# Optimization experiments

Hardware: AMD Instinct MI355X
Metric: run time of the kernel (lower is better)

## Reference

```python
import jax, jax.numpy as jnp
import numpy as np

B, T, C = 8, 2048, 1024
HS = 128           # head_size
N_TERMS = 2
THETA = 10000.0


def _rope_tables(dim, end):
    freqs = 1.0 / (THETA ** (jnp.arange(0, dim, 2, dtype=jnp.float32) / dim))  # [dim/2]
    ang = jnp.arange(end, dtype=jnp.float32)[:, None] * freqs[None, :]          # [end, dim/2]
    return jnp.cos(ang), jnp.sin(ang)


def _apply_rope(x, cos, sin):
    # x: [..., T, D]; pairs are interleaved (x0,x1),(x2,x3),...
    xr = x[..., 0::2]
    xi = x[..., 1::2]
    or_ = xr * cos - xi * sin
    oi = xr * sin + xi * cos
    return jnp.stack([or_, oi], axis=-1).reshape(x.shape)


def setup_inputs() -> dict:
    key = jax.random.key(0)
    ks = jax.random.split(key, 6)
    x = jax.random.normal(ks[0], (B, T, C), dtype=jnp.float32)
    Wq = jax.random.normal(ks[1], (N_TERMS, C, HS), dtype=jnp.float32) * 0.02
    Wk = jax.random.normal(ks[2], (N_TERMS, C, HS), dtype=jnp.float32) * 0.02
    Wv = jax.random.normal(ks[3], (C, 2 * HS), dtype=jnp.float32) * 0.02
    lambda_q = jax.random.normal(ks[4], (N_TERMS, HS), dtype=jnp.float32) * 0.1
    lambda_k = jax.random.normal(ks[5], (N_TERMS, HS), dtype=jnp.float32) * 0.1
    return {"x": x, "Wq": Wq, "Wk": Wk, "Wv": Wv,
            "lambda_q": lambda_q, "lambda_k": lambda_k, "layer_idx": 3}


def reference(x, Wq, Wk, Wv, lambda_q, lambda_k, layer_idx):
    Bx, Tx, Cx = x.shape
    n = Wq.shape[0]
    scale = 1.0 / (HS ** 0.5)

    v = x @ Wv                                   # [B,T,2*HS]
    q = jnp.einsum('btc,ncd->nbtd', x, Wq)       # [n,B,T,HS]
    k = jnp.einsum('btc,ncd->nbtd', x, Wk)

    cos, sin = _rope_tables(HS, Tx)              # [T, HS/2]
    q = _apply_rope(q, cos, sin)
    k = _apply_rope(k, cos, sin)

    att = jnp.einsum('nbtd,nbsd->nbts', q, k) * scale  # [n,B,T,T]
    causal = jnp.tril(jnp.ones((Tx, Tx), dtype=bool))
    att = jnp.where(causal, att, -jnp.inf)
    att = jax.nn.softmax(att, axis=-1)

    # lambda values
    lam_init = 0.8 - 0.6 * jnp.exp(-0.3 * (jnp.float32(layer_idx) - 1.0))
    e = jnp.mean(jnp.exp(lambda_q * lambda_k), axis=-1)         # [n]
    e_prev = jnp.concatenate([jnp.zeros((1,), e.dtype), e[:-1]])
    lam = e - e_prev + lam_init                                 # [n]
    signs = jnp.where(jnp.arange(n) % 2 == 1, -1.0, 1.0)

    diff_att = jnp.einsum('n,nbts->bts', signs * lam, att)      # [B,T,T]
    out = diff_att @ v                                          # [B,T,2*HS]
    return out
```

## Files before the change

### kernel.cpp

```cpp
#include <hip/hip_runtime.h>
#include <math.h>

#define B_DIM 8
#define T_DIM 2048
#define C_DIM 1024
#define HS_DIM 128
#define VD 256
#define M_DIM (B_DIM * T_DIM)
#define QK_ELEMS (M_DIM * HS_DIM)
#define SCALE 0.088388347648318447f
#define LOG_THETA 9.210340371976184f

#define QB_OFF   0u
#define KB_OFF   4194304u
#define VT_OFF   8388608u
#define WT_OFF   12582912u
#define XBH_OFF  13369344u
#define LAM_OFF  21757952u
#define XSPLIT_ELEMS 8388608u

typedef short s8v   __attribute__((ext_vector_type(8)));
typedef float f32x4 __attribute__((ext_vector_type(4)));
typedef float f32x16 __attribute__((ext_vector_type(16)));

__device__ __forceinline__ unsigned int bf16_rne(float f) {
    unsigned int u = __float_as_uint(f);
    return (u + 0x7fffu + ((u >> 16) & 1u)) >> 16;
}
__device__ __forceinline__ unsigned int pack_bf2(float lo, float hi) {
    return bf16_rne(lo) | (bf16_rne(hi) << 16);
}
__device__ __forceinline__ void async_cp16(const unsigned short* g, unsigned short* l) {
    __builtin_amdgcn_global_load_lds(
        (const __attribute__((address_space(1))) unsigned int*)g,
        (__attribute__((address_space(3))) unsigned int*)l, 16, 0, 0);
}

__global__ void lam_kernel(const float* __restrict__ lq, const float* __restrict__ lk,
                           const int* __restrict__ lidx, float* __restrict__ lam_out) {
    int t = threadIdx.x;
    float s0 = expf(lq[t] * lk[t]) + expf(lq[t + 64] * lk[t + 64]);
    float s1 = expf(lq[128 + t] * lk[128 + t]) + expf(lq[192 + t] * lk[192 + t]);
    #pragma unroll
    for (int off = 32; off > 0; off >>= 1) {
        s0 += __shfl_down(s0, off);
        s1 += __shfl_down(s1, off);
    }
    if (t == 0) {
        float e0 = s0 * (1.0f / 128.0f);
        float e1 = s1 * (1.0f / 128.0f);
        float li = 0.8f - 0.6f * expf(-0.3f * ((float)lidx[0] - 1.0f));
        lam_out[0] = e0 + li;
        lam_out[1] = -(e1 - e0 + li);
    }
}

__global__ __launch_bounds__(256) void cast_x_kernel(const float* __restrict__ x,
                                                     unsigned short* __restrict__ lo,
                                                     unsigned short* __restrict__ hi) {
    const size_t i8 = ((size_t)blockIdx.x * 256 + threadIdx.x) * 8;
    float4 a = *(const float4*)(x + i8);
    float4 b = *(const float4*)(x + i8 + 4);
    uint4 u;
    u.x = pack_bf2(a.x, a.y); u.y = pack_bf2(a.z, a.w);
    u.z = pack_bf2(b.x, b.y); u.w = pack_bf2(b.z, b.w);
    unsigned short* dst = (i8 < XSPLIT_ELEMS) ? (lo + i8) : (hi + (i8 - XSPLIT_ELEMS));
    *(uint4*)dst = u;
}

__global__ __launch_bounds__(256) void cast_wt_kernel(
    const float* __restrict__ Wq, const float* __restrict__ Wk,
    const float* __restrict__ Wv, unsigned short* __restrict__ wt) {
    __shared__ float tile[32][33];
    const int t = threadIdx.x;
    const int n0 = blockIdx.x * 32;
    const int k0 = blockIdx.y * 32;
    const int seg = n0 >> 7;
    const int nl = t & 31;
    const int ng = n0 + nl;
    const float* src; int ld;
    if (seg < 2)      { src = Wq + (size_t)seg * (C_DIM * HS_DIM) + (ng & 127); ld = 128; }
    else if (seg < 4) { src = Wk + (size_t)(seg - 2) * (C_DIM * HS_DIM) + (ng & 127); ld = 128; }
    else              { src = Wv + (ng - 512); ld = 256; }
    #pragma unroll
    for (int rep = 0; rep < 4; ++rep) {
        int kl = (t >> 5) + rep * 8;
        tile[kl][nl] = src[(size_t)(k0 + kl) * ld];
    }
    __syncthreads();
    unsigned int* wt32 = (unsigned int*)wt;
    #pragma unroll
    for (int rep = 0; rep < 2; ++rep) {
        int nl2 = (t >> 4) + rep * 16;
        int k2 = (t & 15) * 2;
        unsigned int u = pack_bf2(tile[k2][nl2], tile[k2 + 1][nl2]);
        wt32[((size_t)(n0 + nl2) * 1024 + k0 + k2) >> 1] = u;
    }
}

__global__ __launch_bounds__(256) void gemm_kernel(
    const unsigned short* __restrict__ xlo, const unsigned short* __restrict__ xhi,
    const unsigned short* __restrict__ wt,
    unsigned short* __restrict__ qo, unsigned short* __restrict__ ko,
    unsigned short* __restrict__ vo) {
    __shared__ unsigned short As[128 * 32];
    __shared__ unsigned short Bs[128 * 32];

    const int t = threadIdx.x;
    const int wv = t >> 6, lane = t & 63;
    const int quad = lane >> 4, l15 = lane & 15;
    const int m0 = blockIdx.x * 128;
    const int n0 = blockIdx.y * 128;
    const int wr = wv >> 1, wc = wv & 1;

    const unsigned short* xbase = (m0 < 8192)
        ? (xlo + (size_t)m0 * C_DIM) : (xhi + (size_t)(m0 - 8192) * C_DIM);

    f32x4 acc[4][4];
    #pragma unroll
    for (int i = 0; i < 4; ++i)
        #pragma unroll
        for (int j = 0; j < 4; ++j) acc[i][j] = (f32x4){0.f, 0.f, 0.f, 0.f};

    const int srow = lane >> 2;
    const int skof = (lane & 3) * 8;

    for (int k0 = 0; k0 < C_DIM; k0 += 32) {
        #pragma unroll
        for (int j = 0; j < 2; ++j) {
            const int c = wv * 2 + j;
            async_cp16(xbase + (size_t)(c * 16 + srow) * C_DIM + k0 + skof, As + c * 512);
        }
        #pragma unroll
        for (int j = 0; j < 2; ++j) {
            const int c = wv * 2 + j;
            async_cp16(wt + (size_t)(n0 + c * 16 + srow) * C_DIM + k0 + skof, Bs + c * 512);
        }
        __syncthreads();
        s8v af[4], bf[4];
        #pragma unroll
        for (int i = 0; i < 4; ++i)
            af[i] = *(const s8v*)&As[(wr * 64 + i * 16 + l15) * 32 + quad * 8];
        #pragma unroll
        for (int j = 0; j < 4; ++j)
            bf[j] = *(const s8v*)&Bs[(wc * 64 + j * 16 + l15) * 32 + quad * 8];
        #pragma unroll
        for (int i = 0; i < 4; ++i)
            #pragma unroll
            for (int j = 0; j < 4; ++j)
                acc[i][j] = __builtin_amdgcn_mfma_f32_16x16x32_bf16(af[i], bf[j], acc[i][j], 0, 0, 0);
        __syncthreads();
    }

    const int seg = n0 >> 7;
    if (seg < 4) {
        unsigned short* dstbuf = ((seg < 2) ? qo : ko) + (size_t)(seg & 1) * QK_ELEMS;
        float freqj[4];
        #pragma unroll
        for (int j = 0; j < 4; ++j) {
            const int d = wc * 64 + j * 16 + l15;
            freqj[j] = __expf((float)(d >> 1) * (-LOG_THETA / 64.f));
        }
        const int odd = lane & 1;
        #pragma unroll
        for (int i = 0; i < 4; ++i) {
            #pragma unroll
            for (int e = 0; e < 4; ++e) {
                const int m = m0 + wr * 64 + i * 16 + quad * 4 + e;
                const float trow = (float)(m & (T_DIM - 1));
                unsigned int* p32 = (unsigned int*)(dstbuf + (size_t)m * HS_DIM);
                #pragma unroll
                for (int j = 0; j < 4; ++j) {
                    const int d = wc * 64 + j * 16 + l15;
                    const float val = acc[i][j][e];
                    const float other = __shfl_xor(val, 1);
                    float sn_, cs_;
                    __sincosf(trow * freqj[j], &sn_, &cs_);
                    const float out = val * cs_ + (odd ? other * sn_ : -other * sn_);
                    const float out2 = __shfl_xor(out, 1);
                    if (!odd) p32[d >> 1] = pack_bf2(out, out2);
                }
            }
        }
    } else {
        const int bq = m0 >> 11;
        const int tbase = m0 & (T_DIM - 1);
        unsigned int* vT32 = (unsigned int*)vo;
        #pragma unroll
        for (int j = 0; j < 4; ++j) {
            const int d = (seg - 4) * 128 + wc * 64 + j * 16 + l15;
            const size_t rowbase = (size_t)(bq * VD + d) * (T_DIM / 2);
            #pragma unroll
            for (int i = 0; i < 4; ++i) {
                const int tok = tbase + wr * 64 + i * 16 + quad * 4;
                uint2 u;
                u.x = pack_bf2(acc[i][j][0], acc[i][j][1]);
                u.y = pack_bf2(acc[i][j][2], acc[i][j][3]);
                *(uint2*)&vT32[rowbase + (tok >> 1)] = u;
            }
        }
    }
}

#define KSTR 136
#define VSTR 72
#define PSTR 72
#define OSTR 260
#define K_OFF 0
#define V_OFF 34816
#define P_OFF 71680
#define SM_TOTAL 80896

__global__ __launch_bounds__(256, 2) void attn_kernel(
    const unsigned short* __restrict__ qg, const unsigned short* __restrict__ kg,
    const unsigned short* __restrict__ vg, const float* __restrict__ lam,
    float* __restrict__ outp) {
    __shared__ __align__(16) unsigned char smem[SM_TOTAL];
    unsigned short* Ks = (unsigned short*)(smem + K_OFF);
    unsigned short* Vt = (unsigned short*)(smem + V_OFF);
    unsigned short* Ps = (unsigned short*)(smem + P_OFF);
    float* Ol = (float*)smem;
    float* Lsum = (float*)(smem + P_OFF);

    const int t = threadIdx.x;
    const int id = blockIdx.x;
    const int b = id & 7;
    const int sidx = id >> 3;
    const int strip = (sidx < 32) ? (63 - sidx) : (sidx - 32);
    const int q0 = strip * 32;
    const int nt = (strip >> 1) + 1;

    const int w = t >> 6, lane = t & 63;
    const int l31 = lane & 31, lh = lane >> 5;
    const int term = w & 1;
    const int kh = w >> 1;

    const float cn = lam[term];

    const unsigned short* qrow = qg
        + ((size_t)(term * B_DIM + b) * T_DIM + q0 + l31) * HS_DIM + lh * 8;
    s8v qa[8];
    #pragma unroll
    for (int ks = 0; ks < 8; ++ks)
        qa[ks] = *(const s8v*)(qrow + ks * 16);

    f32x16 o[4];
    #pragma unroll
    for (int dt = 0; dt < 4; ++dt)
        #pragma unroll
        for (int r = 0; r < 16; ++r) o[dt][r] = 0.f;
    float l_acc[16];
    #pragma unroll
    for (int r = 0; r < 16; ++r) l_acc[r] = 0.f;

    for (int it = 0; it < nt; ++it) {
        const int s0 = it * 64;
        #pragma unroll
        for (int rep = 0; rep < 8; ++rep) {
            int idx = t + rep * 256;
            int n = idx >> 10, rem = idx & 1023;
            int r = rem >> 4, seg = rem & 15;
            const uint4 g = *(const uint4*)(kg
                + ((size_t)(n * B_DIM + b) * T_DIM + s0 + r) * HS_DIM + seg * 8);
            *(uint4*)&Ks[(n * 64 + r) * KSTR + seg * 8] = g;
        }
        #pragma unroll
        for (int rep = 0; rep < 8; ++rep) {
            int idx = t + rep * 256;
            int d = idx >> 3, seg = idx & 7;
            const uint4 g = *(const uint4*)(vg
                + ((size_t)(b * VD + d) * T_DIM + s0) + seg * 8);
            *(uint4*)&Vt[d * VSTR + seg * 8] = g;
        }
        __syncthreads();

        f32x16 sc;
        #pragma unroll
        for (int r = 0; r < 16; ++r) sc[r] = 0.f;
        #pragma unroll
        for (int ks = 0; ks < 8; ++ks) {
            s8v kf = *(const s8v*)&Ks[(term * 64 + kh * 32 + l31) * KSTR
                                      + ks * 16 + lh * 8];
            sc = __builtin_amdgcn_mfma_f32_32x32x16_bf16(qa[ks], kf, sc, 0, 0, 0);
        }
        const int key = s0 + kh * 32 + l31;
        #pragma unroll
        for (int r = 0; r < 16; ++r) {
            const int row = (r & 3) + 8 * (r >> 2) + 4 * lh;
            const float p = (key <= q0 + row) ? __expf(sc[r] * SCALE) : 0.f;
            l_acc[r] += p;
            Ps[(term * 32 + row) * PSTR + kh * 32 + l31] = (unsigned short)bf16_rne(p);
        }
        __syncthreads();

        #pragma unroll
        for (int ks = 0; ks < 4; ++ks) {
            s8v pa = *(const s8v*)&Ps[(term * 32 + l31) * PSTR + ks * 16 + lh * 8];
            #pragma unroll
            for (int dt = 0; dt < 4; ++dt) {
                s8v vb = *(const s8v*)&Vt[(kh * 128 + dt * 32 + l31) * VSTR
                                          + ks * 16 + lh * 8];
                o[dt] = __builtin_amdgcn_mfma_f32_32x32x16_bf16(pa, vb, o[dt], 0, 0, 0);
            }
        }
        __syncthreads();
    }

    #pragma unroll
    for (int r = 0; r < 16; ++r) {
        float lt = l_acc[r];
        #pragma unroll
        for (int off = 1; off < 32; off <<= 1) lt += __shfl_xor(lt, off);
        if (l31 == 0) {
            const int row = (r & 3) + 8 * (r >> 2) + 4 * lh;
            Lsum[(term * 2 + kh) * 32 + row] = lt;
        }
    }
    __syncthreads();
    float inv[16];
    #pragma unroll
    for (int r = 0; r < 16; ++r) {
        const int row = (r & 3) + 8 * (r >> 2) + 4 * lh;
        inv[r] = cn / (Lsum[(term * 2 + 0) * 32 + row] + Lsum[(term * 2 + 1) * 32 + row]);
    }

    if (term) {
        #pragma unroll
        for (int dt = 0; dt < 4; ++dt)
            #pragma unroll
            for (int r = 0; r < 16; ++r) {
                const int row = (r & 3) + 8 * (r >> 2) + 4 * lh;
                Ol[row * OSTR + kh * 128 + dt * 32 + l31] = o[dt][r] * inv[r];
            }
    }
    __syncthreads();
    if (!term) {
        #pragma unroll
        for (int dt = 0; dt < 4; ++dt)
            #pragma unroll
            for (int r = 0; r < 16; ++r) {
                const int row = (r & 3) + 8 * (r >> 2) + 4 * lh;
                Ol[row * OSTR + kh * 128 + dt * 32 + l31] += o[dt][r] * inv[r];
            }
    }
    __syncthreads();
    #pragma unroll
    for (int rep = 0; rep < 8; ++rep) {
        int idx = t + rep * 256;
        int row = idx >> 6, c4 = idx & 63;
        float4 val = *(const float4*)&Ol[row * OSTR + c4 * 4];
        *(float4*)&outp[((size_t)(b * T_DIM + q0 + row)) * VD + c4 * 4] = val;
    }
}

extern "C" void kernel_launch(void* const* d_in, const int* in_sizes, int n_in,
                              void* d_out, int out_size, void* d_ws, size_t ws_size,
                              hipStream_t stream) {
    const float* x  = (const float*)d_in[0];
    const float* Wq = (const float*)d_in[1];
    const float* Wk = (const float*)d_in[2];
    const float* Wv = (const float*)d_in[3];
    const float* lq = (const float*)d_in[4];
    const float* lk = (const float*)d_in[5];
    const int* lidx = (const int*)d_in[6];

    unsigned short* ws = (unsigned short*)d_ws;
    unsigned short* qb   = ws + QB_OFF;
    unsigned short* kb   = ws + KB_OFF;
    unsigned short* vTb  = ws + VT_OFF;
    unsigned short* wtb  = ws + WT_OFF;
    unsigned short* xbhi = ws + XBH_OFF;
    float* lamb = (float*)(ws + LAM_OFF);
    unsigned short* xblo = (unsigned short*)d_out;
    (void)ws_size; (void)in_sizes; (void)n_in; (void)out_size;

    lam_kernel<<<dim3(1), dim3(64), 0, stream>>>(lq, lk, lidx, lamb);
    cast_x_kernel<<<dim3(8192), dim3(256), 0, stream>>>(x, xblo, xbhi);
    cast_wt_kernel<<<dim3(24, 32), dim3(256), 0, stream>>>(Wq, Wk, Wv, wtb);
    gemm_kernel<<<dim3(128, 6), dim3(256), 0, stream>>>(xblo, xbhi, wtb, qb, kb, vTb);
    attn_kernel<<<dim3(512), dim3(256), 0, stream>>>(qb, kb, vTb, lamb, (float*)d_out);
}
```

Baseline: 231.7 us.

## Load K and V fragments straight from global into registers, double-buffer P

```diff
diff --git a/kernel.cpp b/kernel.cpp
--- a/kernel.cpp
+++ b/kernel.cpp
@@ -202,25 +202,20 @@
     }
 }
 
-#define KSTR 136
-#define VSTR 72
 #define PSTR 72
+#define PBUF (2 * 32 * PSTR)
 #define OSTR 260
-#define K_OFF 0
-#define V_OFF 34816
-#define P_OFF 71680
-#define SM_TOTAL 80896
+#define L_OFF 18432
+#define SM_TOTAL 33280
 
 __global__ __launch_bounds__(256, 2) void attn_kernel(
     const unsigned short* __restrict__ qg, const unsigned short* __restrict__ kg,
     const unsigned short* __restrict__ vg, const float* __restrict__ lam,
     float* __restrict__ outp) {
     __shared__ __align__(16) unsigned char smem[SM_TOTAL];
-    unsigned short* Ks = (unsigned short*)(smem + K_OFF);
-    unsigned short* Vt = (unsigned short*)(smem + V_OFF);
-    unsigned short* Ps = (unsigned short*)(smem + P_OFF);
+    unsigned short* Ps = (unsigned short*)smem;
+    float* Lsum = (float*)(smem + L_OFF);
     float* Ol = (float*)smem;
-    float* Lsum = (float*)(smem + P_OFF);
 
     const int t = threadIdx.x;
     const int id = blockIdx.x;
@@ -244,6 +239,11 @@
     for (int ks = 0; ks < 8; ++ks)
         qa[ks] = *(const s8v*)(qrow + ks * 16);
 
+    const unsigned short* kbase = kg
+        + ((size_t)(term * B_DIM + b) * T_DIM + kh * 32 + l31) * HS_DIM + lh * 8;
+    const unsigned short* vbase = vg
+        + ((size_t)(b * VD + kh * 128 + l31) * T_DIM) + lh * 8;
+
     f32x16 o[4];
     #pragma unroll
     for (int dt = 0; dt < 4; ++dt)
@@ -253,57 +253,53 @@
     #pragma unroll
     for (int r = 0; r < 16; ++r) l_acc[r] = 0.f;
 
+    s8v kf[8];
+    #pragma unroll
+    for (int ks = 0; ks < 8; ++ks)
+        kf[ks] = *(const s8v*)(kbase + ks * 16);
+
     for (int it = 0; it < nt; ++it) {
         const int s0 = it * 64;
-        #pragma unroll
-        for (int rep = 0; rep < 8; ++rep) {
-            int idx = t + rep * 256;
-            int n = idx >> 10, rem = idx & 1023;
-            int r = rem >> 4, seg = rem & 15;
-            const uint4 g = *(const uint4*)(kg
-                + ((size_t)(n * B_DIM + b) * T_DIM + s0 + r) * HS_DIM + seg * 8);
-            *(uint4*)&Ks[(n * 64 + r) * KSTR + seg * 8] = g;
-        }
-        #pragma unroll
-        for (int rep = 0; rep < 8; ++rep) {
-            int idx = t + rep * 256;
-            int d = idx >> 3, seg = idx & 7;
-            const uint4 g = *(const uint4*)(vg
-                + ((size_t)(b * VD + d) * T_DIM + s0) + seg * 8);
-            *(uint4*)&Vt[d * VSTR + seg * 8] = g;
-        }
-        __syncthreads();
+        unsigned short* Pb = Ps + (it & 1) * PBUF;
+
+        s8v vb[16];
+        #pragma unroll
+        for (int dt = 0; dt < 4; ++dt)
+            #pragma unroll
+            for (int ks = 0; ks < 4; ++ks)
+                vb[dt * 4 + ks] = *(const s8v*)(vbase
+                    + (size_t)dt * 32 * T_DIM + s0 + ks * 16);
 
         f32x16 sc;
         #pragma unroll
         for (int r = 0; r < 16; ++r) sc[r] = 0.f;
         #pragma unroll
-        for (int ks = 0; ks < 8; ++ks) {
-            s8v kf = *(const s8v*)&Ks[(term * 64 + kh * 32 + l31) * KSTR
-                                      + ks * 16 + lh * 8];
-            sc = __builtin_amdgcn_mfma_f32_32x32x16_bf16(qa[ks], kf, sc, 0, 0, 0);
-        }
+        for (int ks = 0; ks < 8; ++ks)
+            sc = __builtin_amdgcn_mfma_f32_32x32x16_bf16(qa[ks], kf[ks], sc, 0, 0, 0);
+
+        const int s0n = (it + 1 < nt) ? (it + 1) * 64 : 0;
+        #pragma unroll
+        for (int ks = 0; ks < 8; ++ks)
+            kf[ks] = *(const s8v*)(kbase + (size_t)s0n * HS_DIM + ks * 16);
+
         const int key = s0 + kh * 32 + l31;
         #pragma unroll
         for (int r = 0; r < 16; ++r) {
             const int row = (r & 3) + 8 * (r >> 2) + 4 * lh;
             const float p = (key <= q0 + row) ? __expf(sc[r] * SCALE) : 0.f;
             l_acc[r] += p;
-            Ps[(term * 32 + row) * PSTR + kh * 32 + l31] = (unsigned short)bf16_rne(p);
+            Pb[(term * 32 + row) * PSTR + kh * 32 + l31] = (unsigned short)bf16_rne(p);
         }
         __syncthreads();
 
         #pragma unroll
         for (int ks = 0; ks < 4; ++ks) {
-            s8v pa = *(const s8v*)&Ps[(term * 32 + l31) * PSTR + ks * 16 + lh * 8];
-            #pragma unroll
-            for (int dt = 0; dt < 4; ++dt) {
-                s8v vb = *(const s8v*)&Vt[(kh * 128 + dt * 32 + l31) * VSTR
-                                          + ks * 16 + lh * 8];
-                o[dt] = __builtin_amdgcn_mfma_f32_32x32x16_bf16(pa, vb, o[dt], 0, 0, 0);
-            }
-        }
-        __syncthreads();
+            s8v pa = *(const s8v*)&Pb[(term * 32 + l31) * PSTR + ks * 16 + lh * 8];
+            #pragma unroll
+            for (int dt = 0; dt < 4; ++dt)
+                o[dt] = __builtin_amdgcn_mfma_f32_32x32x16_bf16(pa, vb[dt * 4 + ks],
+                                                                o[dt], 0, 0, 0);
+        }
     }
 
     #pragma unroll
@@ -323,6 +319,7 @@
         const int row = (r & 3) + 8 * (r >> 2) + 4 * lh;
         inv[r] = cn / (Lsum[(term * 2 + 0) * 32 + row] + Lsum[(term * 2 + 1) * 32 + row]);
     }
+    __syncthreads();
 
     if (term) {
         #pragma unroll
```

After: 295.9 us. 1.28x slower.

## Prefetch next K/V tile into registers during attention MFMA compute

Applied to the files above, without the earlier changes.

```diff
diff --git a/kernel.cpp b/kernel.cpp
--- a/kernel.cpp
+++ b/kernel.cpp
@@ -244,6 +244,20 @@
     for (int ks = 0; ks < 8; ++ks)
         qa[ks] = *(const s8v*)(qrow + ks * 16);
 
+    const unsigned short* ksrc[8]; int kdst[8];
+    const unsigned short* vsrc[8]; int vdst[8];
+    #pragma unroll
+    for (int rep = 0; rep < 8; ++rep) {
+        const int idx = t + rep * 256;
+        const int n = idx >> 10, rem = idx & 1023;
+        const int r = rem >> 4, seg = rem & 15;
+        ksrc[rep] = kg + ((size_t)(n * B_DIM + b) * T_DIM + r) * HS_DIM + seg * 8;
+        kdst[rep] = (n * 64 + r) * KSTR + seg * 8;
+        const int d = idx >> 3, vseg = idx & 7;
+        vsrc[rep] = vg + ((size_t)(b * VD + d) * T_DIM) + vseg * 8;
+        vdst[rep] = d * VSTR + vseg * 8;
+    }
+
     f32x16 o[4];
     #pragma unroll
     for (int dt = 0; dt < 4; ++dt)
@@ -253,36 +267,43 @@
     #pragma unroll
     for (int r = 0; r < 16; ++r) l_acc[r] = 0.f;
 
+    uint4 gk[8], gv[8];
+    #pragma unroll
+    for (int rep = 0; rep < 8; ++rep) {
+        gk[rep] = *(const uint4*)(ksrc[rep]);
+        gv[rep] = *(const uint4*)(vsrc[rep]);
+    }
+    #pragma unroll
+    for (int rep = 0; rep < 8; ++rep) {
+        *(uint4*)&Ks[kdst[rep]] = gk[rep];
+        *(uint4*)&Vt[vdst[rep]] = gv[rep];
+    }
+    __syncthreads();
+
     for (int it = 0; it < nt; ++it) {
         const int s0 = it * 64;
-        #pragma unroll
-        for (int rep = 0; rep < 8; ++rep) {
-            int idx = t + rep * 256;
-            int n = idx >> 10, rem = idx & 1023;
-            int r = rem >> 4, seg = rem & 15;
-            const uint4 g = *(const uint4*)(kg
-                + ((size_t)(n * B_DIM + b) * T_DIM + s0 + r) * HS_DIM + seg * 8);
-            *(uint4*)&Ks[(n * 64 + r) * KSTR + seg * 8] = g;
-        }
-        #pragma unroll
-        for (int rep = 0; rep < 8; ++rep) {
-            int idx = t + rep * 256;
-            int d = idx >> 3, seg = idx & 7;
-            const uint4 g = *(const uint4*)(vg
-                + ((size_t)(b * VD + d) * T_DIM + s0) + seg * 8);
-            *(uint4*)&Vt[d * VSTR + seg * 8] = g;
-        }
-        __syncthreads();
+        const bool has_next = (it + 1) < nt;
+
+        if (has_next) {
+            const int sn = s0 + 64;
+            #pragma unroll
+            for (int rep = 0; rep < 8; ++rep) {
+                gk[rep] = *(const uint4*)(ksrc[rep] + (size_t)sn * HS_DIM);
+                gv[rep] = *(const uint4*)(vsrc[rep] + sn);
+            }
+        }
 
         f32x16 sc;
         #pragma unroll
         for (int r = 0; r < 16; ++r) sc[r] = 0.f;
+        __builtin_amdgcn_s_setprio(1);
         #pragma unroll
         for (int ks = 0; ks < 8; ++ks) {
             s8v kf = *(const s8v*)&Ks[(term * 64 + kh * 32 + l31) * KSTR
                                       + ks * 16 + lh * 8];
             sc = __builtin_amdgcn_mfma_f32_32x32x16_bf16(qa[ks], kf, sc, 0, 0, 0);
         }
+        __builtin_amdgcn_s_setprio(0);
         const int key = s0 + kh * 32 + l31;
         #pragma unroll
         for (int r = 0; r < 16; ++r) {
@@ -293,6 +314,7 @@
         }
         __syncthreads();
 
+        __builtin_amdgcn_s_setprio(1);
         #pragma unroll
         for (int ks = 0; ks < 4; ++ks) {
             s8v pa = *(const s8v*)&Ps[(term * 32 + l31) * PSTR + ks * 16 + lh * 8];
@@ -301,6 +323,16 @@
                 s8v vb = *(const s8v*)&Vt[(kh * 128 + dt * 32 + l31) * VSTR
                                           + ks * 16 + lh * 8];
                 o[dt] = __builtin_amdgcn_mfma_f32_32x32x16_bf16(pa, vb, o[dt], 0, 0, 0);
+            }
+        }
+        __builtin_amdgcn_s_setprio(0);
+        __syncthreads();
+
+        if (has_next) {
+            #pragma unroll
+            for (int rep = 0; rep < 8; ++rep) {
+                *(uint4*)&Ks[kdst[rep]] = gk[rep];
+                *(uint4*)&Vt[vdst[rep]] = gv[rep];
             }
         }
         __syncthreads();
```

Result: slower. 422.5 us (+82.3%).

## Double-buffer K/V tiles with async copies and keep P in registers

Applied to the files above, without the earlier changes.

```diff
diff --git a/kernel.cpp b/kernel.cpp
--- a/kernel.cpp
+++ b/kernel.cpp
@@ -202,25 +202,19 @@
     }
 }
 
-#define KSTR 136
-#define VSTR 72
-#define PSTR 72
+#define KVB 32
+#define BUFB 32768
+#define LS_OFF 65536
+#define SM_TOTAL 65792
 #define OSTR 260
-#define K_OFF 0
-#define V_OFF 34816
-#define P_OFF 71680
-#define SM_TOTAL 80896
 
 __global__ __launch_bounds__(256, 2) void attn_kernel(
     const unsigned short* __restrict__ qg, const unsigned short* __restrict__ kg,
     const unsigned short* __restrict__ vg, const float* __restrict__ lam,
     float* __restrict__ outp) {
     __shared__ __align__(16) unsigned char smem[SM_TOTAL];
-    unsigned short* Ks = (unsigned short*)(smem + K_OFF);
-    unsigned short* Vt = (unsigned short*)(smem + V_OFF);
-    unsigned short* Ps = (unsigned short*)(smem + P_OFF);
+    float* Lsum = (float*)(smem + LS_OFF);
     float* Ol = (float*)smem;
-    float* Lsum = (float*)(smem + P_OFF);
 
     const int t = threadIdx.x;
     const int id = blockIdx.x;
@@ -228,12 +222,12 @@
     const int sidx = id >> 3;
     const int strip = (sidx < 32) ? (63 - sidx) : (sidx - 32);
     const int q0 = strip * 32;
-    const int nt = (strip >> 1) + 1;
+    const int nt = strip + 1;
 
     const int w = t >> 6, lane = t & 63;
     const int l31 = lane & 31, lh = lane >> 5;
     const int term = w & 1;
-    const int kh = w >> 1;
+    const int dh = w >> 1;
 
     const float cn = lam[term];
 
@@ -244,84 +238,122 @@
     for (int ks = 0; ks < 8; ++ks)
         qa[ks] = *(const s8v*)(qrow + ks * 16);
 
+    const unsigned short* ksrcb[4];
+    const unsigned short* vsrcb[4];
+    #pragma unroll
+    for (int rep = 0; rep < 4; ++rep) {
+        const int idx = t + rep * 256;
+        const int kterm = idx >> 9, krow = (idx >> 4) & 31, kslot = idx & 15;
+        const int ksw = kslot ^ (krow & 7);
+        ksrcb[rep] = kg + ((size_t)(kterm * B_DIM + b) * T_DIM + krow) * HS_DIM + ksw * 8;
+        const int j = idx;
+        const int vrow = j >> 3, vslot = j & 7;
+        const int vsw = vslot ^ (vrow & 7);
+        const int vdim = 2 * vrow + (vsw >> 2), vtc = vsw & 3;
+        vsrcb[rep] = vg + ((size_t)(b * VD + vdim)) * T_DIM + vtc * 8;
+    }
+
     f32x16 o[4];
     #pragma unroll
     for (int dt = 0; dt < 4; ++dt)
         #pragma unroll
         for (int r = 0; r < 16; ++r) o[dt][r] = 0.f;
-    float l_acc[16];
-    #pragma unroll
-    for (int r = 0; r < 16; ++r) l_acc[r] = 0.f;
+    float lsc = 0.f;
+
+    {
+        unsigned short* kd = (unsigned short*)(smem) + t * 8;
+        unsigned short* vd = (unsigned short*)(smem + 16384) + t * 8;
+        #pragma unroll
+        for (int rep = 0; rep < 4; ++rep) {
+            async_cp16(ksrcb[rep], kd + rep * 2048);
+            async_cp16(vsrcb[rep], vd + rep * 2048);
+        }
+    }
+    __syncthreads();
 
     for (int it = 0; it < nt; ++it) {
-        const int s0 = it * 64;
-        #pragma unroll
-        for (int rep = 0; rep < 8; ++rep) {
-            int idx = t + rep * 256;
-            int n = idx >> 10, rem = idx & 1023;
-            int r = rem >> 4, seg = rem & 15;
-            const uint4 g = *(const uint4*)(kg
-                + ((size_t)(n * B_DIM + b) * T_DIM + s0 + r) * HS_DIM + seg * 8);
-            *(uint4*)&Ks[(n * 64 + r) * KSTR + seg * 8] = g;
-        }
-        #pragma unroll
-        for (int rep = 0; rep < 8; ++rep) {
-            int idx = t + rep * 256;
-            int d = idx >> 3, seg = idx & 7;
-            const uint4 g = *(const uint4*)(vg
-                + ((size_t)(b * VD + d) * T_DIM + s0) + seg * 8);
-            *(uint4*)&Vt[d * VSTR + seg * 8] = g;
-        }
+        const int s0 = it * KVB;
+        const int c = it & 1;
+        unsigned char* buf = smem + c * BUFB;
+
+        if (it + 1 < nt) {
+            const int sn = s0 + KVB;
+            unsigned char* nbuf = smem + (c ^ 1) * BUFB;
+            unsigned short* kd = (unsigned short*)(nbuf) + t * 8;
+            unsigned short* vd = (unsigned short*)(nbuf + 16384) + t * 8;
+            #pragma unroll
+            for (int rep = 0; rep < 4; ++rep) {
+                async_cp16(ksrcb[rep] + (size_t)sn * HS_DIM, kd + rep * 2048);
+                async_cp16(vsrcb[rep] + sn, vd + rep * 2048);
+            }
+        }
+
+        const unsigned short* Kb = (const unsigned short*)buf;
+        f32x16 sc;
+        #pragma unroll
+        for (int r = 0; r < 16; ++r) sc[r] = 0.f;
+        __builtin_amdgcn_s_setprio(1);
+        #pragma unroll
+        for (int ks = 0; ks < 8; ++ks) {
+            const int slot = (ks * 2 + lh) ^ (l31 & 7);
+            s8v kf = *(const s8v*)&Kb[((term * 32 + l31) * 16 + slot) * 8];
+            sc = __builtin_amdgcn_mfma_f32_32x32x16_bf16(kf, qa[ks], sc, 0, 0, 0);
+        }
+        __builtin_amdgcn_s_setprio(0);
+
+        float p[16];
+        #pragma unroll
+        for (int r = 0; r < 16; ++r) {
+            const int key = s0 + (r & 3) + 8 * (r >> 2) + 4 * lh;
+            p[r] = (key <= q0 + l31) ? __expf(sc[r] * SCALE) : 0.f;
+            lsc += p[r];
+        }
+
+        s8v pa[2];
+        #pragma unroll
+        for (int ks = 0; ks < 2; ++ks) {
+            const unsigned int X0 = pack_bf2(p[8 * ks + 0], p[8 * ks + 1]);
+            const unsigned int X1 = pack_bf2(p[8 * ks + 2], p[8 * ks + 3]);
+            const unsigned int Y0 = pack_bf2(p[8 * ks + 4], p[8 * ks + 5]);
+            const unsigned int Y1 = pack_bf2(p[8 * ks + 6], p[8 * ks + 7]);
+            const unsigned int pX0 = __shfl_xor((int)X0, 32);
+            const unsigned int pX1 = __shfl_xor((int)X1, 32);
+            const unsigned int pY0 = __shfl_xor((int)Y0, 32);
+            const unsigned int pY1 = __shfl_xor((int)Y1, 32);
+            unsigned int wbuf[4];
+            wbuf[0] = lh ? pY0 : X0;
+            wbuf[1] = lh ? pY1 : X1;
+            wbuf[2] = lh ? Y0 : pX0;
+            wbuf[3] = lh ? Y1 : pX1;
+            pa[ks] = *(const s8v*)wbuf;
+        }
+
+        const unsigned short* Vb = (const unsigned short*)(buf + 16384);
+        __builtin_amdgcn_s_setprio(1);
+        #pragma unroll
+        for (int ks = 0; ks < 2; ++ks) {
+            #pragma unroll
+            for (int dt = 0; dt < 4; ++dt) {
+                const int dim = dh * 128 + dt * 32 + l31;
+                const int vrow = dim >> 1;
+                const int slot = ((dim & 1) * 4 + ks * 2 + lh) ^ (vrow & 7);
+                s8v vb = *(const s8v*)&Vb[(vrow * 8 + slot) * 8];
+                o[dt] = __builtin_amdgcn_mfma_f32_32x32x16_bf16(pa[ks], vb, o[dt], 0, 0, 0);
+            }
+        }
+        __builtin_amdgcn_s_setprio(0);
+
         __syncthreads();
-
-        f32x16 sc;
-        #pragma unroll
-        for (int r = 0; r < 16; ++r) sc[r] = 0.f;
-        #pragma unroll
-        for (int ks = 0; ks < 8; ++ks) {
-            s8v kf = *(const s8v*)&Ks[(term * 64 + kh * 32 + l31) * KSTR
-                                      + ks * 16 + lh * 8];
-            sc = __builtin_amdgcn_mfma_f32_32x32x16_bf16(qa[ks], kf, sc, 0, 0, 0);
-        }
-        const int key = s0 + kh * 32 + l31;
-        #pragma unroll
-        for (int r = 0; r < 16; ++r) {
-            const int row = (r & 3) + 8 * (r >> 2) + 4 * lh;
-            const float p = (key <= q0 + row) ? __expf(sc[r] * SCALE) : 0.f;
-            l_acc[r] += p;
-            Ps[(term * 32 + row) * PSTR + kh * 32 + l31] = (unsigned short)bf16_rne(p);
-        }
-        __syncthreads();
-
-        #pragma unroll
-        for (int ks = 0; ks < 4; ++ks) {
-            s8v pa = *(const s8v*)&Ps[(term * 32 + l31) * PSTR + ks * 16 + lh * 8];
-            #pragma unroll
-            for (int dt = 0; dt < 4; ++dt) {
-                s8v vb = *(const s8v*)&Vt[(kh * 128 + dt * 32 + l31) * VSTR
-                                          + ks * 16 + lh * 8];
-                o[dt] = __builtin_amdgcn_mfma_f32_32x32x16_bf16(pa, vb, o[dt], 0, 0, 0);
-            }
-        }
-        __syncthreads();
-    }
-
-    #pragma unroll
-    for (int r = 0; r < 16; ++r) {
-        float lt = l_acc[r];
-        #pragma unroll
-        for (int off = 1; off < 32; off <<= 1) lt += __shfl_xor(lt, off);
-        if (l31 == 0) {
-            const int row = (r & 3) + 8 * (r >> 2) + 4 * lh;
-            Lsum[(term * 2 + kh) * 32 + row] = lt;
-        }
-    }
+    }
+
+    const float ltot = lsc + __shfl_xor(lsc, 32);
+    if (dh == 0 && lh == 0) Lsum[term * 32 + l31] = ltot;
     __syncthreads();
     float inv[16];
     #pragma unroll
     for (int r = 0; r < 16; ++r) {
         const int row = (r & 3) + 8 * (r >> 2) + 4 * lh;
-        inv[r] = cn / (Lsum[(term * 2 + 0) * 32 + row] + Lsum[(term * 2 + 1) * 32 + row]);
+        inv[r] = cn / Lsum[term * 32 + row];
     }
 
     if (term) {
@@ -330,7 +362,7 @@
             #pragma unroll
             for (int r = 0; r < 16; ++r) {
                 const int row = (r & 3) + 8 * (r >> 2) + 4 * lh;
-                Ol[row * OSTR + kh * 128 + dt * 32 + l31] = o[dt][r] * inv[r];
+                Ol[row * OSTR + dh * 128 + dt * 32 + l31] = o[dt][r] * inv[r];
             }
     }
     __syncthreads();
@@ -340,7 +372,7 @@
             #pragma unroll
             for (int r = 0; r < 16; ++r) {
                 const int row = (r & 3) + 8 * (r >> 2) + 4 * lh;
-                Ol[row * OSTR + kh * 128 + dt * 32 + l31] += o[dt][r] * inv[r];
+                Ol[row * OSTR + dh * 128 + dt * 32 + l31] += o[dt][r] * inv[r];
             }
     }
     __syncthreads();
```

After: 255.3 us. 10.2% more time.
